# Optimization experiments

Hardware: AMD Instinct MI355X
Metric: run time of the kernel (lower is better)

## Reference

```python
import jax, jax.numpy as jnp
import numpy as np

MAX_PATCH = 40   # static pad >= max points per grid cell + 1 (grid/fake token slot)
NUM_HEADS = 8


def _cumcount_1d(cell):
    """For each element, number of earlier elements with the same cell id. O(U log U) via stable sort."""
    U = cell.shape[0]
    order = jnp.argsort(cell)              # stable
    sc = cell[order]
    pos = jnp.arange(U)
    new_run = jnp.concatenate([jnp.ones((1,), bool), sc[1:] != sc[:-1]])
    run_start = jax.lax.associative_scan(jnp.maximum, jnp.where(new_run, pos, 0))  # cummax
    return jnp.zeros(U, jnp.int32).at[order].set((pos - run_start).astype(jnp.int32))


def setup_inputs() -> dict:
    key = jax.random.key(0)
    ks = jax.random.split(key, 10)
    B, U, E = 8, 8192, 256
    n = m = 32
    coords = jnp.linspace(0.0, 1.0, n)
    grid = jnp.stack(jnp.meshgrid(coords, coords, indexing='ij'), axis=-1)  # [n,m,2]
    xc_on_grid = jnp.broadcast_to(grid, (B, n, m, 2))
    xc_off_grid = jax.random.uniform(ks[0], (B, U, 2))
    zc_off_grid = jax.random.normal(ks[1], (B, U, E), jnp.float32)
    zc_on_grid = jax.random.normal(ks[2], (B, n, m, E), jnp.float32)
    latents = jax.random.normal(ks[3], (n, m, E), jnp.float32)
    fake_embedding = jax.random.normal(ks[4], (E,), jnp.float32)
    sc = 1.0 / np.sqrt(E)
    Wq = jax.random.normal(ks[5], (E, E), jnp.float32) * sc
    Wk = jax.random.normal(ks[6], (E, E), jnp.float32) * sc
    Wv = jax.random.normal(ks[7], (E, E), jnp.float32) * sc
    Wo = jax.random.normal(ks[8], (E, E), jnp.float32) * sc
    return dict(xc_off_grid=xc_off_grid, xc_on_grid=xc_on_grid,
                zc_off_grid=zc_off_grid, zc_on_grid=zc_on_grid,
                latents=latents, fake_embedding=fake_embedding,
                Wq=Wq, Wk=Wk, Wv=Wv, Wo=Wo, ignore_on_grid=0)


def reference(xc_off_grid, xc_on_grid, zc_off_grid, zc_on_grid,
              latents, fake_embedding, Wq, Wk, Wv, Wo, ignore_on_grid):
    B, U, E = zc_off_grid.shape
    _, n, m, _ = xc_on_grid.shape
    S = n * m
    MP = MAX_PATCH

    # nearest grid cell per off-grid point (uniform grid on [0,1], n points/dim)
    row = jnp.clip(jnp.round(xc_off_grid[..., 0] * (n - 1)).astype(jnp.int32), 0, n - 1)
    col = jnp.clip(jnp.round(xc_off_grid[..., 1] * (m - 1)).astype(jnp.int32), 0, m - 1)
    cell = row * m + col                                    # [B,U]

    cumcount = jax.vmap(_cumcount_1d)(cell)                 # [B,U]
    counts = jnp.zeros((B, S), jnp.int32).at[jnp.arange(B)[:, None], cell].add(1)

    # scatter off-grid tokens into padded per-cell buckets [B*S, MP, E]
    bs = (jnp.arange(B)[:, None] * S + cell).reshape(-1)
    slot = jnp.where(cumcount < MP - 1, cumcount, MP).reshape(-1)  # overflow -> dropped
    gs = jnp.zeros((B * S, MP, E), zc_off_grid.dtype)
    gs = gs.at[bs, slot].set(zc_off_grid.reshape(B * U, E), mode='drop')

    # last slot: on-grid token (or fake embedding when ignore_on_grid)
    if ignore_on_grid:
        last = jnp.broadcast_to(fake_embedding, (B * S, E))
    else:
        last = zc_on_grid.reshape(B * S, E)
    gs = gs.at[:, MP - 1].set(last)

    slots = jnp.arange(MP)
    valid = (slots[None, :] < counts.reshape(-1)[:, None]) | (slots == MP - 1)  # [B*S, MP]

    # masked MHCA: one latent query per cell attends over its bucket
    H = NUM_HEADS
    hd = E // H
    lat = jnp.broadcast_to(latents.reshape(1, S, E), (B, S, E)).reshape(B * S, E)
    q = (lat @ Wq).reshape(B * S, H, hd)
    k = (gs @ Wk).reshape(B * S, MP, H, hd)
    v = (gs @ Wv).reshape(B * S, MP, H, hd)
    scores = jnp.einsum('bhd,bphd->bhp', q, k) / np.sqrt(hd)
    scores = jnp.where(valid[:, None, :], scores, -jnp.inf)
    attn = jax.nn.softmax(scores, axis=-1)
    out = jnp.einsum('bhp,bphd->bhd', attn, v).reshape(B * S, E) @ Wo
    z_grid = out.reshape(B, n, m, E)
    return (xc_on_grid, z_grid)
```

## Files before the change

### kernel.cpp

```cpp
#include <hip/hip_runtime.h>
#include <hip/hip_bf16.h>

#define B_   8
#define U_   8192
#define E_   256
#define N_   32
#define S_   1024
#define MP_  40
#define H_   8
#define NLIST 39
#define NCAP  35
#define NTOKMAX 36
#define GCELLS (B_*S_)
#define KDIM  (H_*E_)
#define GEMMBLK 512

typedef unsigned short ushort_t;
using bf16x8 = __attribute__((ext_vector_type(8))) short;
using f32x4  = __attribute__((ext_vector_type(4))) float;

#define WS_COUNTS 0u
#define WS_LISTS  32768u
#define WS_LATB   1310720u
#define WS_WQKT   1835008u
#define WS_WVOT   2883584u
#define WS_QKB    3932160u
#define WS_W      8126464u

__device__ inline unsigned pk2(float a, float b) {
    unsigned r;
    asm("v_cvt_pk_bf16_f32 %0, %1, %2" : "=v"(r) : "v"(a), "v"(b));
    return r;
}
__device__ inline float ubf(ushort_t u) {
    unsigned v = (unsigned)u << 16;
    return *(float*)&v;
}

__global__ __launch_bounds__(256)
void prep(const float* __restrict__ latents,
          const float* __restrict__ Wq, const float* __restrict__ Wk,
          const float* __restrict__ Wv, const float* __restrict__ Wo,
          const float* __restrict__ xc_on, float* __restrict__ out,
          int* __restrict__ counts,
          ushort_t* __restrict__ latb, ushort_t* __restrict__ wqkT,
          ushort_t* __restrict__ wvoT) {
    __shared__ float smem[10496];
    int blk = blockIdx.x, tid = threadIdx.x;

    if (blk < 128) {
        int i = blk * 256 + tid;
        const float4* src = (const float4*)latents + 2 * i;
        float4 a = src[0], c = src[1];
        uint4 o;
        o.x = pk2(a.x, a.y); o.y = pk2(a.z, a.w);
        o.z = pk2(c.x, c.y); o.w = pk2(c.z, c.w);
        ((uint4*)latb)[i] = o;
    } else if (blk < 192) {
        int b2 = blk - 128, h = b2 >> 3, e0 = (b2 & 7) * 32;
        float* wq_s = smem;
        for (int i = tid; i < 8192; i += 256) {
            int f = i >> 5, d = i & 31;
            wq_s[f * 33 + d] = Wq[f * E_ + h * 32 + d];
        }
        __syncthreads();
        int e = e0 + (tid & 31), fg = tid >> 5;
        float wk[32];
        #pragma unroll
        for (int d4 = 0; d4 < 8; ++d4) {
            float4 v = *(const float4*)(Wk + (size_t)e * E_ + h * 32 + d4 * 4);
            wk[d4*4] = v.x; wk[d4*4+1] = v.y; wk[d4*4+2] = v.z; wk[d4*4+3] = v.w;
        }
        const float invs = 0.17677669529663687f;
        ushort_t* dst = wqkT + (size_t)(h * E_ + e) * E_ + fg * 32;
        for (int q8 = 0; q8 < 4; ++q8) {
            float t8[8];
            #pragma unroll
            for (int k = 0; k < 8; ++k) {
                int f = fg * 32 + q8 * 8 + k;
                float acc = 0.f;
                #pragma unroll
                for (int d = 0; d < 32; ++d) acc += wq_s[f * 33 + d] * wk[d];
                t8[k] = acc * invs;
            }
            uint4 o;
            o.x = pk2(t8[0], t8[1]); o.y = pk2(t8[2], t8[3]);
            o.z = pk2(t8[4], t8[5]); o.w = pk2(t8[6], t8[7]);
            *(uint4*)(dst + q8 * 8) = o;
        }
    } else if (blk < 224) {
        int b3 = blk - 192, h = b3 >> 2, e0p = (b3 & 3) * 64;
        float* wv_s = smem;
        float* wo_s = smem + 8448;
        for (int i = tid; i < 8192; i += 256) {
            int e = i >> 5, d = i & 31;
            wv_s[e * 33 + d] = Wv[e * E_ + h * 32 + d];
        }
        for (int i = tid; i < 2048; i += 256) {
            int d = i >> 6, el = i & 63;
            wo_s[i] = Wo[(h * 32 + d) * E_ + e0p + el];
        }
        __syncthreads();
        int erow = tid & 63, eg = tid >> 6;
        float wor[32];
        #pragma unroll
        for (int d = 0; d < 32; ++d) wor[d] = wo_s[d * 64 + erow];
        ushort_t* dst = wvoT + (size_t)(e0p + erow) * KDIM + h * E_ + eg * 64;
        for (int q8 = 0; q8 < 8; ++q8) {
            float t8[8];
            #pragma unroll
            for (int k = 0; k < 8; ++k) {
                int e = eg * 64 + q8 * 8 + k;
                float acc = 0.f;
                #pragma unroll
                for (int d = 0; d < 32; ++d) acc += wv_s[e * 33 + d] * wor[d];
                t8[k] = acc;
            }
            uint4 o;
            o.x = pk2(t8[0], t8[1]); o.y = pk2(t8[2], t8[3]);
            o.z = pk2(t8[4], t8[5]); o.w = pk2(t8[6], t8[7]);
            *(uint4*)(dst + q8 * 8) = o;
        }
    } else {
        int i = (blk - 224) * 256 + tid;
        ((float4*)out)[i] = ((const float4*)xc_on)[i];
        if (i < 2048) ((int4*)counts)[i] = make_int4(0, 0, 0, 0);
    }
}

template<bool BF16OUT, bool DO_BUILD>
__global__ __launch_bounds__(256)
void gemm_k(const ushort_t* __restrict__ A, const ushort_t* __restrict__ BT,
            void* __restrict__ Cv, int Kdim, int Ndim, int lgNTX,
            const float* __restrict__ xc_off, int* __restrict__ counts,
            int* __restrict__ lists) {
    if (DO_BUILD && (int)blockIdx.x >= GEMMBLK) {
        int t = ((int)blockIdx.x - GEMMBLK) * 256 + threadIdx.x;
        float x = xc_off[2 * t], y = xc_off[2 * t + 1];
        int row = (int)rintf(x * 31.f); row = min(max(row, 0), 31);
        int col = (int)rintf(y * 31.f); col = min(max(col, 0), 31);
        int b = t >> 13;
        int g = b * S_ + row * N_ + col;
        int old = atomicAdd(&counts[g], 1);
        if (old < NLIST) lists[g * NLIST + old] = t & (U_ - 1);
        return;
    }
    constexpr int LDB = 72;
    __shared__ ushort_t As[64 * LDB];
    __shared__ ushort_t Bs[64 * LDB];
    int tid = threadIdx.x;
    int idx = blockIdx.x;
    idx = (idx & 7) * (GEMMBLK >> 3) + (idx >> 3);
    int nTX = 1 << lgNTX;
    int m0 = (idx >> lgNTX) * 64, n0 = (idx & (nTX - 1)) * 64;

    int wave = tid >> 6, lane = tid & 63;
    int wr = wave >> 1, wc = wave & 1;
    int l15 = lane & 15, lg = lane >> 4;

    f32x4 acc[2][2];
    #pragma unroll
    for (int m = 0; m < 2; ++m)
        #pragma unroll
        for (int n = 0; n < 2; ++n)
            acc[m][n] = (f32x4){0.f, 0.f, 0.f, 0.f};

    int r0 = tid >> 3, u0 = tid & 7;
    int r1 = r0 + 32, u1 = u0;

    const ushort_t* pa0 = A  + (size_t)(m0 + r0) * Kdim + u0 * 8;
    const ushort_t* pa1 = A  + (size_t)(m0 + r1) * Kdim + u1 * 8;
    const ushort_t* pb0 = BT + (size_t)(n0 + r0) * Kdim + u0 * 8;
    const ushort_t* pb1 = BT + (size_t)(n0 + r1) * Kdim + u1 * 8;

    uint4 a0 = *(const uint4*)(pa0);
    uint4 a1 = *(const uint4*)(pa1);
    uint4 b0 = *(const uint4*)(pb0);
    uint4 b1 = *(const uint4*)(pb1);

    for (int kt = 0; kt < Kdim; kt += 64) {
        __syncthreads();
        *(uint4*)(As + r0 * LDB + u0 * 8) = a0;
        *(uint4*)(As + r1 * LDB + u1 * 8) = a1;
        *(uint4*)(Bs + r0 * LDB + u0 * 8) = b0;
        *(uint4*)(Bs + r1 * LDB + u1 * 8) = b1;
        __syncthreads();
        if (kt + 64 < Kdim) {
            a0 = *(const uint4*)(pa0 + kt + 64);
            a1 = *(const uint4*)(pa1 + kt + 64);
            b0 = *(const uint4*)(pb0 + kt + 64);
            b1 = *(const uint4*)(pb1 + kt + 64);
        }
        #pragma unroll
        for (int kk = 0; kk < 2; ++kk) {
            bf16x8 af[2], bfr[2];
            #pragma unroll
            for (int m = 0; m < 2; ++m)
                af[m] = *(const bf16x8*)(As + (wr * 32 + m * 16 + l15) * LDB + (kk * 4 + lg) * 8);
            #pragma unroll
            for (int n = 0; n < 2; ++n)
                bfr[n] = *(const bf16x8*)(Bs + (wc * 32 + n * 16 + l15) * LDB + (kk * 4 + lg) * 8);
            #pragma unroll
            for (int m = 0; m < 2; ++m)
                #pragma unroll
                for (int n = 0; n < 2; ++n)
                    acc[m][n] = __builtin_amdgcn_mfma_f32_16x16x32_bf16(
                        af[m], bfr[n], acc[m][n], 0, 0, 0);
        }
    }
    #pragma unroll
    for (int m = 0; m < 2; ++m)
        #pragma unroll
        for (int n = 0; n < 2; ++n)
            #pragma unroll
            for (int q = 0; q < 4; ++q) {
                int row = m0 + wr * 32 + m * 16 + lg * 4 + q;
                int col = n0 + wc * 32 + n * 16 + l15;
                if (BF16OUT) {
                    __hip_bfloat16 hb = __float2bfloat16(acc[m][n][q]);
                    ((ushort_t*)Cv)[(size_t)row * Ndim + col] = *(ushort_t*)&hb;
                } else {
                    ((float*)Cv)[(size_t)row * Ndim + col] = acc[m][n][q];
                }
            }
}

__global__ __launch_bounds__(256, 8)
void pool_cells(const float* __restrict__ zc_off, const float* __restrict__ zc_on,
                const float* __restrict__ fake, const ushort_t* __restrict__ qkb,
                const int* __restrict__ counts, const int* __restrict__ lists,
                const int* __restrict__ ig_p, ushort_t* __restrict__ wout) {
    __shared__ __align__(16) ushort_t tok[NTOKMAX * E_];
    __shared__ float sc[H_ * 48];

    int g = blockIdx.x, s = g & (S_ - 1), b = g >> 10, tid = threadIdx.x;
    int h = tid >> 5, j = tid & 31;

    int cnt = min(counts[g], NCAP);
    int ntok = cnt + 1, ig = ig_p[0];
    const float* lastrow = ig ? fake : zc_on + (size_t)g * E_;

    {
        uint4* t4 = (uint4*)tok;
        for (int i = tid; i < ntok * 32; i += 256) {
            int p = i >> 5, q = i & 31;
            const float* src = (p < cnt)
                ? zc_off + ((size_t)b * U_ + lists[g * NLIST + p]) * E_
                : lastrow;
            float4 x = *(const float4*)(src + q * 8);
            float4 y = *(const float4*)(src + q * 8 + 4);
            uint4 o;
            o.x = pk2(x.x, x.y); o.y = pk2(x.z, x.w);
            o.z = pk2(y.x, y.y); o.w = pk2(y.z, y.w);
            t4[((p << 5) + q) ^ (p & 7)] = o;
        }
    }
    __syncthreads();

    if (tid < 64) {
        int l15 = tid & 15, lg = tid >> 4;
        bf16x8 af[8];
        const ushort_t* qrow = qkb + (size_t)s * KDIM + l15 * E_ + lg * 8;
        #pragma unroll
        for (int kk = 0; kk < 8; ++kk)
            af[kk] = *(const bf16x8*)(qrow + kk * 32);
        const bf16x8* tv = (const bf16x8*)tok;
        int ntiles = (ntok + 15) >> 4;
        for (int t = 0; t < ntiles; ++t) {
            f32x4 acc = (f32x4){0.f, 0.f, 0.f, 0.f};
            int row = t * 16 + l15;
            int rc = row < NTOKMAX ? row : NTOKMAX - 1;
            #pragma unroll
            for (int kk = 0; kk < 8; ++kk) {
                bf16x8 bfr = tv[((rc << 5) + (kk << 2) + lg) ^ (rc & 7)];
                acc = __builtin_amdgcn_mfma_f32_16x16x32_bf16(af[kk], bfr, acc, 0, 0, 0);
            }
            if (lg < 2) {
                #pragma unroll
                for (int q = 0; q < 4; ++q)
                    sc[(lg * 4 + q) * 48 + t * 16 + l15] = acc[q];
            }
        }
    }
    __syncthreads();

    {
        float v0 = (j < ntok) ? sc[h * 48 + j] : -1e30f;
        float v1 = (j + 32 < ntok) ? sc[h * 48 + j + 32] : -1e30f;
        float mx = fmaxf(v0, v1);
        #pragma unroll
        for (int off = 16; off; off >>= 1) mx = fmaxf(mx, __shfl_xor(mx, off, 32));
        float e0 = (j < ntok) ? __expf(v0 - mx) : 0.f;
        float e1 = (j + 32 < ntok) ? __expf(v1 - mx) : 0.f;
        float sm = e0 + e1;
        #pragma unroll
        for (int off = 16; off; off >>= 1) sm += __shfl_xor(sm, off, 32);
        float inv = 1.f / sm;
        if (j < ntok)      sc[h * 48 + j] = e0 * inv;
        if (j + 32 < ntok) sc[h * 48 + j + 32] = e1 * inv;
    }

    float acc[8];
    #pragma unroll
    for (int k = 0; k < 8; ++k) acc[k] = 0.f;
    const bf16x8* tv2 = (const bf16x8*)tok;
    for (int p = 0; p < ntok; ++p) {
        float a = sc[h * 48 + p];
        bf16x8 t8 = tv2[((p << 5) + j) ^ (p & 7)];
        #pragma unroll
        for (int k = 0; k < 8; ++k) acc[k] += a * ubf((ushort_t)t8[k]);
    }
    uint4 o;
    o.x = pk2(acc[0], acc[1]); o.y = pk2(acc[2], acc[3]);
    o.z = pk2(acc[4], acc[5]); o.w = pk2(acc[6], acc[7]);
    ((uint4*)(wout + (size_t)g * KDIM))[tid] = o;
}

extern "C" void kernel_launch(void* const* d_in, const int* in_sizes, int n_in,
                              void* d_out, int out_size, void* d_ws, size_t ws_size,
                              hipStream_t stream) {
    const float* xc_off  = (const float*)d_in[0];
    const float* xc_on   = (const float*)d_in[1];
    const float* zc_off  = (const float*)d_in[2];
    const float* zc_on   = (const float*)d_in[3];
    const float* latents = (const float*)d_in[4];
    const float* fake    = (const float*)d_in[5];
    const float* Wq      = (const float*)d_in[6];
    const float* Wk      = (const float*)d_in[7];
    const float* Wv      = (const float*)d_in[8];
    const float* Wo      = (const float*)d_in[9];
    const int*   ig      = (const int*)d_in[10];
    float* out = (float*)d_out;

    char* ws = (char*)d_ws;
    int*      counts = (int*)(ws + WS_COUNTS);
    int*      lists  = (int*)(ws + WS_LISTS);
    ushort_t* latb   = (ushort_t*)(ws + WS_LATB);
    ushort_t* wqkT   = (ushort_t*)(ws + WS_WQKT);
    ushort_t* wvoT   = (ushort_t*)(ws + WS_WVOT);
    ushort_t* qkb    = (ushort_t*)(ws + WS_QKB);
    ushort_t* w      = (ushort_t*)(ws + WS_W);

    const int PASS = B_ * N_ * N_ * 2;

    prep<<<240, 256, 0, stream>>>(latents, Wq, Wk, Wv, Wo, xc_on, out,
                                  counts, latb, wqkT, wvoT);

    gemm_k<true, true><<<GEMMBLK + 256, 256, 0, stream>>>(
        latb, wqkT, qkb, 256, KDIM, 5, xc_off, counts, lists);

    pool_cells<<<GCELLS, 256, 0, stream>>>(zc_off, zc_on, fake, qkb,
                                           counts, lists, ig, w);

    gemm_k<false, false><<<GEMMBLK, 256, 0, stream>>>(
        w, wvoT, out + PASS, KDIM, E_, 2, nullptr, nullptr, nullptr);
}
```

Measured before the change: 70.50 us.

## Process two cells per pooling block and prefetch second cell's tokens into registers

After: 75.45 us. +7.0%, slower.

```diff
diff --git a/kernel.cpp b/kernel.cpp
--- a/kernel.cpp
+++ b/kernel.cpp
@@ -225,42 +225,13 @@
             }
 }
 
-__global__ __launch_bounds__(256, 8)
-void pool_cells(const float* __restrict__ zc_off, const float* __restrict__ zc_on,
-                const float* __restrict__ fake, const ushort_t* __restrict__ qkb,
-                const int* __restrict__ counts, const int* __restrict__ lists,
-                const int* __restrict__ ig_p, ushort_t* __restrict__ wout) {
-    __shared__ __align__(16) ushort_t tok[NTOKMAX * E_];
-    __shared__ float sc[H_ * 48];
-
-    int g = blockIdx.x, s = g & (S_ - 1), b = g >> 10, tid = threadIdx.x;
-    int h = tid >> 5, j = tid & 31;
-
-    int cnt = min(counts[g], NCAP);
-    int ntok = cnt + 1, ig = ig_p[0];
-    const float* lastrow = ig ? fake : zc_on + (size_t)g * E_;
-
-    {
-        uint4* t4 = (uint4*)tok;
-        for (int i = tid; i < ntok * 32; i += 256) {
-            int p = i >> 5, q = i & 31;
-            const float* src = (p < cnt)
-                ? zc_off + ((size_t)b * U_ + lists[g * NLIST + p]) * E_
-                : lastrow;
-            float4 x = *(const float4*)(src + q * 8);
-            float4 y = *(const float4*)(src + q * 8 + 4);
-            uint4 o;
-            o.x = pk2(x.x, x.y); o.y = pk2(x.z, x.w);
-            o.z = pk2(y.x, y.y); o.w = pk2(y.z, y.w);
-            t4[((p << 5) + q) ^ (p & 7)] = o;
-        }
-    }
-    __syncthreads();
-
+__device__ __forceinline__ void cell_compute(
+    ushort_t* tok, float* sc, const ushort_t* qrow_base,
+    int ntok, int tid, int h, int j, ushort_t* wout_g) {
     if (tid < 64) {
         int l15 = tid & 15, lg = tid >> 4;
         bf16x8 af[8];
-        const ushort_t* qrow = qkb + (size_t)s * KDIM + l15 * E_ + lg * 8;
+        const ushort_t* qrow = qrow_base + l15 * E_ + lg * 8;
         #pragma unroll
         for (int kk = 0; kk < 8; ++kk)
             af[kk] = *(const bf16x8*)(qrow + kk * 32);
@@ -313,7 +284,106 @@
     uint4 o;
     o.x = pk2(acc[0], acc[1]); o.y = pk2(acc[2], acc[3]);
     o.z = pk2(acc[4], acc[5]); o.w = pk2(acc[6], acc[7]);
-    ((uint4*)(wout + (size_t)g * KDIM))[tid] = o;
+    ((uint4*)wout_g)[tid] = o;
+}
+
+__global__ __launch_bounds__(256, 8)
+void pool_cells2(const float* __restrict__ zc_off, const float* __restrict__ zc_on,
+                 const float* __restrict__ fake, const ushort_t* __restrict__ qkb,
+                 const int* __restrict__ counts, const int* __restrict__ lists,
+                 const int* __restrict__ ig_p, ushort_t* __restrict__ wout) {
+    __shared__ __align__(16) ushort_t tok[NTOKMAX * E_];
+    __shared__ float sc[H_ * 48];
+
+    int blk = blockIdx.x;
+    int s = blk & (S_ - 1), bh = blk >> 10;
+    int gA = bh * S_ + s, gB = (bh + 4) * S_ + s;
+    int tid = threadIdx.x;
+    int h = tid >> 5, j = tid & 31;
+
+    int cntA = min(counts[gA], NCAP);
+    int cntB = min(counts[gB], NCAP);
+    int ig = ig_p[0];
+    int ntokA = cntA + 1, ntokB = cntB + 1;
+    const float* lastA = ig ? fake : zc_on + (size_t)gA * E_;
+    const float* lastB = ig ? fake : zc_on + (size_t)gB * E_;
+
+    uint4* t4 = (uint4*)tok;
+
+    for (int i = tid; i < ntokA * 32; i += 256) {
+        int p = i >> 5, q = i & 31;
+        const float* src = (p < cntA)
+            ? zc_off + ((size_t)bh * U_ + lists[gA * NLIST + p]) * E_
+            : lastA;
+        float4 x = ((const float4*)src)[2 * q];
+        float4 y = ((const float4*)src)[2 * q + 1];
+        uint4 o;
+        o.x = pk2(x.x, x.y); o.y = pk2(x.z, x.w);
+        o.z = pk2(y.x, y.y); o.w = pk2(y.z, y.w);
+        t4[((p << 5) + q) ^ (p & 7)] = o;
+    }
+
+    float4 xB0, yB0, xB1, yB1, xB2, yB2;
+    int pB0 = tid >> 5,        qB0 = tid & 31;
+    int pB1 = (tid + 256) >> 5, qB1 = qB0;
+    int pB2 = (tid + 512) >> 5, qB2 = qB0;
+    {
+        if (pB0 < ntokB) {
+            const float* sp = (pB0 < cntB)
+                ? zc_off + ((size_t)(bh + 4) * U_ + lists[gB * NLIST + pB0]) * E_ : lastB;
+            xB0 = ((const float4*)sp)[2 * qB0]; yB0 = ((const float4*)sp)[2 * qB0 + 1];
+        }
+        if (pB1 < ntokB) {
+            const float* sp = (pB1 < cntB)
+                ? zc_off + ((size_t)(bh + 4) * U_ + lists[gB * NLIST + pB1]) * E_ : lastB;
+            xB1 = ((const float4*)sp)[2 * qB1]; yB1 = ((const float4*)sp)[2 * qB1 + 1];
+        }
+        if (pB2 < ntokB) {
+            const float* sp = (pB2 < cntB)
+                ? zc_off + ((size_t)(bh + 4) * U_ + lists[gB * NLIST + pB2]) * E_ : lastB;
+            xB2 = ((const float4*)sp)[2 * qB2]; yB2 = ((const float4*)sp)[2 * qB2 + 1];
+        }
+    }
+    __syncthreads();
+
+    cell_compute(tok, sc, qkb + (size_t)s * KDIM, ntokA, tid, h, j,
+                 wout + (size_t)gA * KDIM);
+    __syncthreads();
+
+    if (pB0 < ntokB) {
+        uint4 o;
+        o.x = pk2(xB0.x, xB0.y); o.y = pk2(xB0.z, xB0.w);
+        o.z = pk2(yB0.x, yB0.y); o.w = pk2(yB0.z, yB0.w);
+        t4[((pB0 << 5) + qB0) ^ (pB0 & 7)] = o;
+    }
+    if (pB1 < ntokB) {
+        uint4 o;
+        o.x = pk2(xB1.x, xB1.y); o.y = pk2(xB1.z, xB1.w);
+        o.z = pk2(yB1.x, yB1.y); o.w = pk2(yB1.z, yB1.w);
+        t4[((pB1 << 5) + qB1) ^ (pB1 & 7)] = o;
+    }
+    if (pB2 < ntokB) {
+        uint4 o;
+        o.x = pk2(xB2.x, xB2.y); o.y = pk2(xB2.z, xB2.w);
+        o.z = pk2(yB2.x, yB2.y); o.w = pk2(yB2.z, yB2.w);
+        t4[((pB2 << 5) + qB2) ^ (pB2 & 7)] = o;
+    }
+    for (int i = 768 + tid; i < ntokB * 32; i += 256) {
+        int p = i >> 5, q = i & 31;
+        const float* src = (p < cntB)
+            ? zc_off + ((size_t)(bh + 4) * U_ + lists[gB * NLIST + p]) * E_
+            : lastB;
+        float4 x = ((const float4*)src)[2 * q];
+        float4 y = ((const float4*)src)[2 * q + 1];
+        uint4 o;
+        o.x = pk2(x.x, x.y); o.y = pk2(x.z, x.w);
+        o.z = pk2(y.x, y.y); o.w = pk2(y.z, y.w);
+        t4[((p << 5) + q) ^ (p & 7)] = o;
+    }
+    __syncthreads();
+
+    cell_compute(tok, sc, qkb + (size_t)s * KDIM, ntokB, tid, h, j,
+                 wout + (size_t)gB * KDIM);
 }
 
 extern "C" void kernel_launch(void* const* d_in, const int* in_sizes, int n_in,
@@ -349,8 +419,8 @@
     gemm_k<true, true><<<GEMMBLK + 256, 256, 0, stream>>>(
         latb, wqkT, qkb, 256, KDIM, 5, xc_off, counts, lists);
 
-    pool_cells<<<GCELLS, 256, 0, stream>>>(zc_off, zc_on, fake, qkb,
-                                           counts, lists, ig, w);
+    pool_cells2<<<GCELLS / 2, 256, 0, stream>>>(zc_off, zc_on, fake, qkb,
+                                                counts, lists, ig, w);
 
     gemm_k<false, false><<<GEMMBLK, 256, 0, stream>>>(
         w, wvoT, out + PASS, KDIM, E_, 2, nullptr, nullptr, nullptr);
```
